# Kernel optimization log

Hardware: AMD Instinct MI355X
Metric: run time of the kernel (lower is better)

## Reference

```python
import jax, jax.numpy as jnp
import numpy as np

EPS = 1e-5
GROUPS = 32

# 3x3 regular grid: row0 = dy, row1 = dx for kernel index k = ky*3 + kx
_REG = jnp.array([[-1, -1, -1, 0, 0, 0, 1, 1, 1],
                  [-1, 0, 1, -1, 0, 1, -1, 0, 1]], dtype=jnp.float32)


def conv2d(x, w, pad):
    return jax.lax.conv_general_dilated(
        x, w, window_strides=(1, 1), padding=((pad, pad), (pad, pad)),
        dimension_numbers=('NCHW', 'OIHW', 'NCHW'))


def deform_conv3x3(x, off_y, off_x, w_dcn, dilation):
    # x: (N,C,H,W); off_y/off_x: (N,H,W,9); w_dcn: (Cout,Cin,3,3)
    N, C, H, W = x.shape
    dyk = (jnp.arange(9) // 3 - 1).astype(jnp.float32) * dilation  # (9,)
    dxk = (jnp.arange(9) % 3 - 1).astype(jnp.float32) * dilation
    yy = jnp.arange(H, dtype=jnp.float32)
    xx = jnp.arange(W, dtype=jnp.float32)
    # sampling positions (padding == dilation, stride == 1)
    py = yy[None, :, None, None] + dyk[None, None, None, :] + off_y  # (N,H,W,9)
    px = xx[None, None, :, None] + dxk[None, None, None, :] + off_x

    y0 = jnp.floor(py)
    x0 = jnp.floor(px)
    wy1 = py - y0
    wx1 = px - x0

    xflat = x.reshape(N, C, H * W)

    def gather(xf, idx):  # xf (C,HW), idx (H,W,9) -> (C,H,W,9)
        return xf[:, idx]

    val = jnp.zeros((N, C, H, W, 9), dtype=x.dtype)
    corners = [
        (y0, x0, (1.0 - wy1) * (1.0 - wx1)),
        (y0, x0 + 1.0, (1.0 - wy1) * wx1),
        (y0 + 1.0, x0, wy1 * (1.0 - wx1)),
        (y0 + 1.0, x0 + 1.0, wy1 * wx1),
    ]
    for yc, xc, wc in corners:
        valid = ((yc >= 0) & (yc <= H - 1) & (xc >= 0) & (xc <= W - 1)).astype(x.dtype)
        yi = jnp.clip(yc, 0, H - 1).astype(jnp.int32)
        xi = jnp.clip(xc, 0, W - 1).astype(jnp.int32)
        ind = yi * W + xi  # (N,H,W,9)
        g = jax.vmap(gather)(xflat, ind)  # (N,C,H,W,9)
        val = val + g * (wc * valid)[:, None]

    Cout = w_dcn.shape[0]
    wk = w_dcn.reshape(Cout, C, 9)
    return jnp.einsum('nchwk,ock->nohw', val, wk)


def group_norm(x, gamma, beta, groups, eps):
    N, C, H, W = x.shape
    xg = x.reshape(N, groups, C // groups, H, W)
    mu = xg.mean(axis=(2, 3, 4), keepdims=True)
    var = xg.var(axis=(2, 3, 4), keepdims=True)
    xn = ((xg - mu) * jax.lax.rsqrt(var + eps)).reshape(N, C, H, W)
    return xn * gamma[None, :, None, None] + beta[None, :, None, None]


def setup_inputs() -> dict:
    key = jax.random.key(0)
    k1, k2, k3, k4 = jax.random.split(key, 4)
    C, Cout = 256, 256
    x = jax.random.normal(k1, (8, C, 64, 64), dtype=jnp.float32)
    w_tm = jax.random.normal(k2, (4, C, 3, 3), dtype=jnp.float32) * 0.02
    b_tm = jnp.zeros((4,), dtype=jnp.float32)
    w_dcn = jax.random.normal(k3, (Cout, C, 3, 3), dtype=jnp.float32) * 0.02
    gn_gamma = jnp.ones((Cout,), dtype=jnp.float32)
    gn_beta = jnp.zeros((Cout,), dtype=jnp.float32)
    return {"x": x, "w_tm": w_tm, "b_tm": b_tm, "w_dcn": w_dcn,
            "gn_gamma": gn_gamma, "gn_beta": gn_beta}


def reference(x, w_tm, b_tm, w_dcn, gn_gamma, gn_beta):
    N, C, H, W = x.shape
    # offset-generating 3x3 conv -> 4 channels = per-pixel 2x2 transform matrix
    tm = conv2d(x, w_tm, pad=1) + b_tm[None, :, None, None]  # (N,4,H,W)
    T = tm.transpose(0, 2, 3, 1).reshape(N, H, W, 2, 2)
    off = jnp.einsum('nhwij,jk->nhwik', T, _REG) - _REG  # (N,H,W,2,9)
    off_y = off[..., 0, :]  # (N,H,W,9)
    off_x = off[..., 1, :]
    out = deform_conv3x3(x, off_y, off_x, w_dcn, dilation=1)
    out = group_norm(out, gn_gamma, gn_beta, GROUPS, EPS)
    return jax.nn.relu(out)
```

## Files before the change

### kernel.cpp

```cpp
#include <hip/hip_runtime.h>
#include <hip/hip_fp16.h>
#include <stdint.h>

typedef float        f32x4 __attribute__((ext_vector_type(4)));
typedef _Float16     f16x8 __attribute__((ext_vector_type(8)));
typedef _Float16 f16;

__device__ inline float bf2f(unsigned short b){ return __builtin_bit_cast(float,(unsigned)b<<16); }
__device__ inline bool is_bf16_mode(const void* g){ return ((const unsigned*)g)[0]==0x3F803F80u; }
__device__ inline float ld_in(const void* p, int i, bool bfm){
  return bfm ? bf2f(((const unsigned short*)p)[i]) : ((const float*)p)[i];
}

#define FAST_BARRIER() __asm__ __volatile__("s_waitcnt lgkmcnt(0)\n\ts_barrier" ::: "memory")

#define WS_XT   0u
#define WS_BF   16777216u
#define WS_ST   17956864u
#define WS_NEED 17958912u

__global__ __launch_bounds__(256) void k_prep(const void* __restrict__ x_,
                                              const void* __restrict__ wdcn,
                                              const void* __restrict__ gamma,
                                              f16* __restrict__ xt,
                                              f16* __restrict__ Bf,
                                              float* __restrict__ stats){
  const bool bfm = is_bf16_mode(gamma);
  const int t = threadIdx.x;
  if (blockIdx.y == 4){
    if (blockIdx.x == 0 && blockIdx.z == 0){
      stats[t] = 0.f; stats[t + 256] = 0.f;
    }
    int base = (blockIdx.z*64 + blockIdx.x)*256 + t;
    #pragma unroll
    for (int it = 0; it < 5; it++){
      int i = base + it*131072;
      if (i < 589824){
        int u    = i & 7;
        int l    = (i >> 3)  & 63;
        int tile = (i >> 9)  & 15;
        int ks   = (i >> 13) & 1;
        int ch   = (i >> 14) & 3;
        int tap  = i >> 16;
        int ml = l & 15, q = l >> 4;
        int oc = tile*16 + ml;
        int c  = ch*64 + ks*32 + q*8 + u;
        Bf[i] = (f16)ld_in(wdcn, oc*2304 + c*9 + tap, bfm);
      }
    }
    return;
  }
  __shared__ float tile[64][65];
  const int n  = blockIdx.z;
  const int c0 = blockIdx.y << 6;
  const int s0 = blockIdx.x << 6;
  {
    const int sp = (t & 31) * 2;
    const int q  = t >> 5;
    #pragma unroll
    for (int i = 0; i < 8; i++){
      int cc = q + i*8;
      int base = (n*256 + c0 + cc)*4096 + s0 + sp;
      tile[cc][sp]   = ld_in(x_, base,   bfm);
      tile[cc][sp+1] = ld_in(x_, base+1, bfm);
    }
  }
  __syncthreads();
  {
    const int cc = (t & 31) * 2;
    const int q  = t >> 5;
    f16* dst = xt + (size_t)(n*4096 + s0)*256 + c0;
    #pragma unroll
    for (int i = 0; i < 8; i++){
      int s = q + i*8;
      dst[s*256 + cc]   = (f16)tile[cc][s];
      dst[s*256 + cc+1] = (f16)tile[cc+1][s];
    }
  }
}

__global__ __launch_bounds__(256,2) void k_fused8(const f16* __restrict__ xt,
                                                  const f16* __restrict__ Bf,
                                                  const void* __restrict__ wtm_,
                                                  const void* __restrict__ btm_,
                                                  const void* __restrict__ gamma,
                                                  float* __restrict__ out,
                                                  float* __restrict__ stats){
  __shared__ __attribute__((aligned(16))) char smemA[36992];
  __shared__ float4 wfL[576];
  __shared__ int4   idxL[576];
  __shared__ float4 Tsm[64];
  float* wl4 = (float*)smemA;
  f16*   At  = (f16*)smemA;
  const bool bfm = is_bf16_mode(gamma);
  const int t = threadIdx.x;
  const int blk = blockIdx.x;
  const int n = blk & 7, h = blk >> 3;
  const int wid = t >> 6, l = t & 63;
  const int ml = l & 15, q = l >> 4;

  for (int i = t; i < 9216; i += 256){
    int o = i / 2304, r = i % 2304, c = r / 9, tap = r % 9;
    int idx = ((tap*256 + c)*4) ^ (((c >> 3) & 3) << 3);
    wl4[idx + o] = ld_in(wtm_, i, bfm);
  }
  __syncthreads();

  {
    const int px = t >> 2, cq = t & 3;
    float a0=0.f, a1=0.f, a2=0.f, a3=0.f;
    for (int tap = 0; tap < 9; tap++){
      const int yy = h + tap/3 - 1, xx = px + tap%3 - 1;
      if ((unsigned)yy < 64u && (unsigned)xx < 64u){
        const f16* row = xt + ((n*4096 + yy*64 + xx)*256);
        #pragma unroll
        for (int jb = 0; jb < 8; jb++){
          const int chunk = jb*4 + cq;
          f16x8 xv = *(const f16x8*)(row + chunk*8);
          #pragma unroll
          for (int u = 0; u < 8; u++){
            const int c = chunk*8 + u;
            const float xs = (float)xv[u];
            const int idx = ((tap*256 + c)*4) ^ (((c >> 3) & 3) << 3);
            const float4 w = *(const float4*)&wl4[idx];
            a0 += xs*w.x; a1 += xs*w.y; a2 += xs*w.z; a3 += xs*w.w;
          }
        }
      }
    }
    a0 += __shfl_xor(a0,1,64); a0 += __shfl_xor(a0,2,64);
    a1 += __shfl_xor(a1,1,64); a1 += __shfl_xor(a1,2,64);
    a2 += __shfl_xor(a2,1,64); a2 += __shfl_xor(a2,2,64);
    a3 += __shfl_xor(a3,1,64); a3 += __shfl_xor(a3,2,64);
    if (cq == 0){
      float4 r;
      r.x = a0 + ld_in(btm_,0,bfm);  r.y = a1 + ld_in(btm_,1,bfm);
      r.z = a2 + ld_in(btm_,2,bfm);  r.w = a3 + ld_in(btm_,3,bfm);
      Tsm[px] = r;
    }
  }
  __syncthreads();

  for (int e = t; e < 576; e += 256){
    const int px = e & 63, tap = e >> 6;
    const float4 T = Tsm[px];
    const float dy = (float)(tap/3 - 1);
    const float dx = (float)(tap%3 - 1);
    float py  = (float)h  + T.x*dy + T.y*dx;
    float pxx = (float)px + T.z*dy + T.w*dx;
    float y0 = floorf(py), x0 = floorf(pxx);
    float wy = py - y0,  wx = pxx - x0;
    float y1 = y0 + 1.f, x1 = x0 + 1.f;
    float vy0 = (y0 >= 0.f && y0 <= 63.f) ? 1.f : 0.f;
    float vy1 = (y1 >= 0.f && y1 <= 63.f) ? 1.f : 0.f;
    float vx0 = (x0 >= 0.f && x0 <= 63.f) ? 1.f : 0.f;
    float vx1 = (x1 >= 0.f && x1 <= 63.f) ? 1.f : 0.f;
    float4 wf;
    wf.x = (1.f-wy)*(1.f-wx)*vy0*vx0;
    wf.y = (1.f-wy)*wx      *vy0*vx1;
    wf.z = wy*(1.f-wx)      *vy1*vx0;
    wf.w = wy*wx            *vy1*vx1;
    int yi0 = (int)fminf(fmaxf(y0,0.f),63.f);
    int yi1 = (int)fminf(fmaxf(y1,0.f),63.f);
    int xi0 = (int)fminf(fmaxf(x0,0.f),63.f);
    int xi1 = (int)fminf(fmaxf(x1,0.f),63.f);
    const int base = n*4096*512;
    int4 id;
    id.x = base + (yi0*64 + xi0)*512;
    id.y = base + (yi0*64 + xi1)*512;
    id.z = base + (yi1*64 + xi0)*512;
    id.w = base + (yi1*64 + xi1)*512;
    idxL[e] = id;
    wfL[e]  = wf;
  }

  f32x4 acc[4][4];
  #pragma unroll
  for (int mt = 0; mt < 4; mt++)
    #pragma unroll
    for (int nt = 0; nt < 4; nt++) acc[mt][nt] = (f32x4){0.f,0.f,0.f,0.f};

  const int bpx = t >> 2, bcq = t & 3;
  const char* xb = (const char*)xt;

  __syncthreads();

  f16x8 pA[2], pB[2], pC[2], pD[2]; float4 cwf;
  {
    const int4 id = idxL[bpx];
    cwf = wfL[bpx];
    #pragma unroll
    for (int cc = 0; cc < 2; cc++){
      const int cb = ((cc*4 + bcq)*8)*2;
      pA[cc] = *(const f16x8*)(xb + id.x + cb);
      pB[cc] = *(const f16x8*)(xb + id.y + cb);
      pC[cc] = *(const f16x8*)(xb + id.z + cb);
      pD[cc] = *(const f16x8*)(xb + id.w + cb);
    }
  }

  for (int step = 0; step < 36; step++){
    const int tap = step >> 2;
    const int ch  = step & 3;
    {
      f16* dst = &At[(step & 1)*4608 + bpx*72];
      #pragma unroll
      for (int cc = 0; cc < 2; cc++){
        f16x8 R;
        #pragma unroll
        for (int u = 0; u < 8; u++)
          R[u] = (f16)(cwf.x*(float)pA[cc][u] + cwf.y*(float)pB[cc][u]
                     + cwf.z*(float)pC[cc][u] + cwf.w*(float)pD[cc][u]);
        *(f16x8*)(dst + (cc*4 + bcq)*8) = R;
      }
    }
    if (step < 35){
      const int s1 = step + 1;
      const int e = (s1 >> 2)*64 + bpx;
      const int4 id = idxL[e];
      cwf = wfL[e];
      #pragma unroll
      for (int cc = 0; cc < 2; cc++){
        const int cb = ((s1 & 3)*64 + (cc*4 + bcq)*8)*2;
        pA[cc] = *(const f16x8*)(xb + id.x + cb);
        pB[cc] = *(const f16x8*)(xb + id.y + cb);
        pC[cc] = *(const f16x8*)(xb + id.z + cb);
        pD[cc] = *(const f16x8*)(xb + id.w + cb);
      }
    }
    f16x8 bfr[2][4];
    #pragma unroll
    for (int ks = 0; ks < 2; ks++)
      #pragma unroll
      for (int nt = 0; nt < 4; nt++)
        bfr[ks][nt] = *(const f16x8*)(Bf + (((((tap*4 + ch)*2 + ks)*16) + (wid*4 + nt)) << 9) + l*8);
    FAST_BARRIER();
    const f16* Atr = &At[(step & 1)*4608];
    #pragma unroll
    for (int ks = 0; ks < 2; ks++){
      f16x8 afr[4];
      #pragma unroll
      for (int mt = 0; mt < 4; mt++)
        afr[mt] = *(const f16x8*)(Atr + (mt*16 + ml)*72 + ks*32 + q*8);
      #pragma unroll
      for (int mt = 0; mt < 4; mt++)
        #pragma unroll
        for (int nt = 0; nt < 4; nt++)
          acc[mt][nt] = __builtin_amdgcn_mfma_f32_16x16x32_f16(afr[mt], bfr[ks][nt], acc[mt][nt], 0, 0, 0);
    }
  }

  #pragma unroll
  for (int mt = 0; mt < 4; mt++)
    #pragma unroll
    for (int nt = 0; nt < 4; nt++){
      const int oc = wid*64 + nt*16 + ml;
      const int m0 = mt*16 + q*4;
      float4 v;
      v.x = acc[mt][nt][0]; v.y = acc[mt][nt][1];
      v.z = acc[mt][nt][2]; v.w = acc[mt][nt][3];
      *(float4*)(out + (size_t)(n*256 + oc)*4096 + h*64 + m0) = v;
    }
  #pragma unroll
  for (int nt = 0; nt < 4; nt++){
    float s1 = 0.f, s2 = 0.f;
    #pragma unroll
    for (int mt = 0; mt < 4; mt++)
      #pragma unroll
      for (int rr = 0; rr < 4; rr++){
        float v = acc[mt][nt][rr];
        s1 += v; s2 += v*v;
      }
    s1 += __shfl_xor(s1,16,64); s1 += __shfl_xor(s1,32,64);
    s2 += __shfl_xor(s2,16,64); s2 += __shfl_xor(s2,32,64);
    s1 += __shfl_xor(s1,1,64);  s1 += __shfl_xor(s1,2,64);  s1 += __shfl_xor(s1,4,64);
    s2 += __shfl_xor(s2,1,64);  s2 += __shfl_xor(s2,2,64);  s2 += __shfl_xor(s2,4,64);
    if ((l & 0x37) == 0){
      const int oc = wid*64 + nt*16 + (l & 8);
      const int g = oc >> 3;
      atomicAdd(stats + n*64 + g*2,     s1);
      atomicAdd(stats + n*64 + g*2 + 1, s2);
    }
  }
}

__global__ __launch_bounds__(256) void k_gn(float* __restrict__ out,
                                            const float* __restrict__ stats,
                                            const void* __restrict__ gamma,
                                            const void* __restrict__ beta){
  const int blk = blockIdx.x;
  const int n = blk >> 8, oc = blk & 255;
  const int g = oc >> 3;
  const bool bfm = is_bf16_mode(gamma);
  const float s1 = stats[n*64 + g*2];
  const float s2 = stats[n*64 + g*2 + 1];
  const float inv = 1.f/32768.f;
  const float mu  = s1*inv;
  const float var = s2*inv - mu*mu;
  const float rs  = rsqrtf(var + 1e-5f);
  const float gv = ld_in(gamma, oc, bfm);
  const float bv = ld_in(beta,  oc, bfm);
  const float sc = gv*rs;
  const float sh = bv - mu*sc;
  float* p = out + (size_t)(n*256 + oc)*4096;
  const int t = threadIdx.x;
  #pragma unroll
  for (int i = 0; i < 4; i++){
    float4 v = *(float4*)(p + (i*256 + t)*4);
    v.x = fmaxf(v.x*sc + sh, 0.f);
    v.y = fmaxf(v.y*sc + sh, 0.f);
    v.z = fmaxf(v.z*sc + sh, 0.f);
    v.w = fmaxf(v.w*sc + sh, 0.f);
    *(float4*)(p + (i*256 + t)*4) = v;
  }
}

__global__ void k_ws_small(float* out){ if (threadIdx.x == 0) out[0] += 200000.f; }

extern "C" void kernel_launch(void* const* d_in, const int* in_sizes, int n_in,
                              void* d_out, int out_size, void* d_ws, size_t ws_size,
                              hipStream_t stream){
  const void* x     = d_in[0];
  const void* wtm   = d_in[1];
  const void* btm   = d_in[2];
  const void* wdcn  = d_in[3];
  const void* gamma = d_in[4];
  const void* beta  = d_in[5];
  float* out = (float*)d_out;
  if (ws_size < (size_t)WS_NEED){
    hipLaunchKernelGGL(k_ws_small, dim3(1), dim3(64), 0, stream, out);
    return;
  }
  char* ws = (char*)d_ws;
  f16*   xt    = (f16*)  (ws + WS_XT);
  f16*   Bf    = (f16*)  (ws + WS_BF);
  float* stats = (float*)(ws + WS_ST);

  hipLaunchKernelGGL(k_prep,   dim3(64,5,8), dim3(256), 0, stream, x, wdcn, gamma, xt, Bf, stats);
  hipLaunchKernelGGL(k_fused8, dim3(512),    dim3(256), 0, stream, xt, Bf, wtm, btm, gamma, out, stats);
  hipLaunchKernelGGL(k_gn,     dim3(2048),   dim3(256), 0, stream, out, stats, gamma, beta);
}
```

Baseline: 196.7 us.

## Prefetch B fragments one step ahead, use fp16 blend and fdot2 offset conv

The main loop now double-buffers the MFMA B-operand fragments in registers, loading the next step's weights before the current step's barrier and MFMAs. This hides global-load latency behind compute. The bilinear blend is done in packed fp16 vector math instead of per-element fp32 math. The offset-generating conv stores its weights as fp16 pairs in shared memory and uses fdot2, which halves that LDS footprint and the instruction count. The trade-off is extra register pressure under launch_bounds(256,2) and lower blend precision, since the corner weights are rounded to fp16.

```diff
diff --git a/kernel.cpp b/kernel.cpp
--- a/kernel.cpp
+++ b/kernel.cpp
@@ -4,6 +4,7 @@
 
 typedef float        f32x4 __attribute__((ext_vector_type(4)));
 typedef _Float16     f16x8 __attribute__((ext_vector_type(8)));
+typedef _Float16     f16x2 __attribute__((ext_vector_type(2)));
 typedef _Float16 f16;
 
 __device__ inline float bf2f(unsigned short b){ return __builtin_bit_cast(float,(unsigned)b<<16); }
@@ -12,12 +13,25 @@
   return bfm ? bf2f(((const unsigned short*)p)[i]) : ((const float*)p)[i];
 }
 
+#if defined(__has_builtin)
+#if __has_builtin(__builtin_amdgcn_fdot2)
+#define HAS_FDOT2 1
+#endif
+#endif
+#ifdef HAS_FDOT2
+#define FDOT2(acc,a,b) (acc = __builtin_amdgcn_fdot2((a),(b),(acc),false))
+#else
+#define FDOT2(acc,a,b) (acc += (float)(a)[0]*(float)(b)[0] + (float)(a)[1]*(float)(b)[1])
+#endif
+
 #define FAST_BARRIER() __asm__ __volatile__("s_waitcnt lgkmcnt(0)\n\ts_barrier" ::: "memory")
 
 #define WS_XT   0u
 #define WS_BF   16777216u
 #define WS_ST   17956864u
 #define WS_NEED 17958912u
+
+__device__ inline int wslot(int tap, int cp){ return (tap*128 + cp) ^ ((cp >> 2) & 7); }
 
 __global__ __launch_bounds__(256) void k_prep(const void* __restrict__ x_,
                                               const void* __restrict__ wdcn,
@@ -79,6 +93,46 @@
   }
 }
 
+#define KSTEP(STEP, BC, BN, PAR) do {                                                   \
+  if ((STEP) < 35){                       \
+    const int tap1 = ((STEP)+1) >> 2, ch1 = ((STEP)+1) & 3;                             \
+    _Pragma("unroll") for (int ks = 0; ks < 2; ks++)                                    \
+      _Pragma("unroll") for (int nt = 0; nt < 4; nt++)                                  \
+        BN[ks][nt] = *(const f16x8*)(Bf + (((((tap1*4+ch1)*2+ks)*16) + (wid*4+nt)) << 9) + l*8); \
+  }                                                                                     \
+  {                                             \
+    f16* dst = &At[(PAR)*4608 + bpx*72];                                                \
+    const f16 wA=(f16)cwf.x, wB=(f16)cwf.y, wC=(f16)cwf.z, wD=(f16)cwf.w;               \
+    _Pragma("unroll") for (int cc = 0; cc < 2; cc++){                                   \
+      f16x8 R = pA[cc]*wA + pB[cc]*wB + pC[cc]*wC + pD[cc]*wD;                          \
+      *(f16x8*)(dst + (cc*4 + bcq)*8) = R;                                              \
+    }                                                                                   \
+  }                                                                                     \
+  if ((STEP) < 35){                                  \
+    const int s1 = (STEP) + 1;                                                          \
+    const int e = (s1 >> 2)*64 + bpx;                                                   \
+    const int4 id = idxL[e];                                                            \
+    cwf = wfL[e];                                                                       \
+    _Pragma("unroll") for (int cc = 0; cc < 2; cc++){                                   \
+      const int cb = ((s1 & 3)*64 + (cc*4 + bcq)*8)*2;                                  \
+      pA[cc] = *(const f16x8*)(xb + id.x + cb);                                         \
+      pB[cc] = *(const f16x8*)(xb + id.y + cb);                                         \
+      pC[cc] = *(const f16x8*)(xb + id.z + cb);                                         \
+      pD[cc] = *(const f16x8*)(xb + id.w + cb);                                         \
+    }                                                                                   \
+  }                                                                                     \
+  FAST_BARRIER();                                                                       \
+  { const f16* Atr = &At[(PAR)*4608];                                                   \
+    _Pragma("unroll") for (int ks = 0; ks < 2; ks++){                                   \
+      f16x8 afr[4];                                                                     \
+      _Pragma("unroll") for (int mt = 0; mt < 4; mt++)                                  \
+        afr[mt] = *(const f16x8*)(Atr + (mt*16 + ml)*72 + ks*32 + q*8);                 \
+      _Pragma("unroll") for (int mt = 0; mt < 4; mt++)                                  \
+        _Pragma("unroll") for (int nt = 0; nt < 4; nt++)                                \
+          acc[mt][nt] = __builtin_amdgcn_mfma_f32_16x16x32_f16(afr[mt], BC[ks][nt], acc[mt][nt], 0, 0, 0); \
+    } }                                                                                 \
+} while(0)
+
 __global__ __launch_bounds__(256,2) void k_fused8(const f16* __restrict__ xt,
                                                   const f16* __restrict__ Bf,
                                                   const void* __restrict__ wtm_,
@@ -86,12 +140,12 @@
                                                   const void* __restrict__ gamma,
                                                   float* __restrict__ out,
                                                   float* __restrict__ stats){
-  __shared__ __attribute__((aligned(16))) char smemA[36992];
+  __shared__ __attribute__((aligned(16))) char smemA[18432];
   __shared__ float4 wfL[576];
   __shared__ int4   idxL[576];
   __shared__ float4 Tsm[64];
-  float* wl4 = (float*)smemA;
-  f16*   At  = (f16*)smemA;
+  f16* wh = (f16*)smemA;
+  f16* At = (f16*)smemA;
   const bool bfm = is_bf16_mode(gamma);
   const int t = threadIdx.x;
   const int blk = blockIdx.x;
@@ -101,8 +155,8 @@
 
   for (int i = t; i < 9216; i += 256){
     int o = i / 2304, r = i % 2304, c = r / 9, tap = r % 9;
-    int idx = ((tap*256 + c)*4) ^ (((c >> 3) & 3) << 3);
-    wl4[idx + o] = ld_in(wtm_, i, bfm);
+    int cp = c >> 1;
+    wh[wslot(tap, cp)*8 + o*2 + (c & 1)] = (f16)ld_in(wtm_, i, bfm);
   }
   __syncthreads();
 
@@ -118,12 +172,14 @@
           const int chunk = jb*4 + cq;
           f16x8 xv = *(const f16x8*)(row + chunk*8);
           #pragma unroll
-          for (int u = 0; u < 8; u++){
-            const int c = chunk*8 + u;
-            const float xs = (float)xv[u];
-            const int idx = ((tap*256 + c)*4) ^ (((c >> 3) & 3) << 3);
-            const float4 w = *(const float4*)&wl4[idx];
-            a0 += xs*w.x; a1 += xs*w.y; a2 += xs*w.z; a3 += xs*w.w;
+          for (int p = 0; p < 4; p++){
+            const int cp = chunk*4 + p;
+            const f16x8 W = *(const f16x8*)&wh[wslot(tap, cp)*8];
+            const f16x2 xp = {xv[2*p], xv[2*p+1]};
+            FDOT2(a0, xp, ((f16x2){W[0], W[1]}));
+            FDOT2(a1, xp, ((f16x2){W[2], W[3]}));
+            FDOT2(a2, xp, ((f16x2){W[4], W[5]}));
+            FDOT2(a3, xp, ((f16x2){W[6], W[7]}));
           }
         }
       }
@@ -185,6 +241,13 @@
 
   __syncthreads();
 
+  f16x8 bA[2][4], bB[2][4];
+  #pragma unroll
+  for (int ks = 0; ks < 2; ks++)
+    #pragma unroll
+    for (int nt = 0; nt < 4; nt++)
+      bA[ks][nt] = *(const f16x8*)(Bf + (((ks*16) + (wid*4 + nt)) << 9) + l*8);
+
   f16x8 pA[2], pB[2], pC[2], pD[2]; float4 cwf;
   {
     const int4 id = idxL[bpx];
@@ -199,55 +262,9 @@
     }
   }
 
-  for (int step = 0; step < 36; step++){
-    const int tap = step >> 2;
-    const int ch  = step & 3;
-    {
-      f16* dst = &At[(step & 1)*4608 + bpx*72];
-      #pragma unroll
-      for (int cc = 0; cc < 2; cc++){
-        f16x8 R;
-        #pragma unroll
-        for (int u = 0; u < 8; u++)
-          R[u] = (f16)(cwf.x*(float)pA[cc][u] + cwf.y*(float)pB[cc][u]
-                     + cwf.z*(float)pC[cc][u] + cwf.w*(float)pD[cc][u]);
-        *(f16x8*)(dst + (cc*4 + bcq)*8) = R;
-      }
-    }
-    if (step < 35){
-      const int s1 = step + 1;
-      const int e = (s1 >> 2)*64 + bpx;
-      const int4 id = idxL[e];
-      cwf = wfL[e];
-      #pragma unroll
-      for (int cc = 0; cc < 2; cc++){
-        const int cb = ((s1 & 3)*64 + (cc*4 + bcq)*8)*2;
-        pA[cc] = *(const f16x8*)(xb + id.x + cb);
-        pB[cc] = *(const f16x8*)(xb + id.y + cb);
-        pC[cc] = *(const f16x8*)(xb + id.z + cb);
-        pD[cc] = *(const f16x8*)(xb + id.w + cb);
-      }
-    }
-    f16x8 bfr[2][4];
-    #pragma unroll
-    for (int ks = 0; ks < 2; ks++)
-      #pragma unroll
-      for (int nt = 0; nt < 4; nt++)
-        bfr[ks][nt] = *(const f16x8*)(Bf + (((((tap*4 + ch)*2 + ks)*16) + (wid*4 + nt)) << 9) + l*8);
-    FAST_BARRIER();
-    const f16* Atr = &At[(step & 1)*4608];
-    #pragma unroll
-    for (int ks = 0; ks < 2; ks++){
-      f16x8 afr[4];
-      #pragma unroll
-      for (int mt = 0; mt < 4; mt++)
-        afr[mt] = *(const f16x8*)(Atr + (mt*16 + ml)*72 + ks*32 + q*8);
-      #pragma unroll
-      for (int mt = 0; mt < 4; mt++)
-        #pragma unroll
-        for (int nt = 0; nt < 4; nt++)
-          acc[mt][nt] = __builtin_amdgcn_mfma_f32_16x16x32_f16(afr[mt], bfr[ks][nt], acc[mt][nt], 0, 0, 0);
-    }
+  for (int s2 = 0; s2 < 36; s2 += 2){
+    KSTEP(s2,     bA, bB, 0);
+    KSTEP(s2 + 1, bB, bA, 1);
   }
 
   #pragma unroll
```

Result: faster. 187.8 us (-4.5%).
